# Performance work log

Hardware: AMD Instinct MI355X
Metric: run time of the kernel (lower is better)

The kernel has to match this reference:

```python
import jax, jax.numpy as jnp
import numpy as np

N_NODES = 100000


def _hetero_block(x, ei_t, ei_i, Wt, bt, Wi, bi, Wr, br):
    """ResidualGeneralHeteroConvBlock: per-edge-type linear message passing,
    'add' aggregation for temp_previous, 'mean' for intersects, summed across
    edge types, plus linear residual, ReLU."""
    n = x.shape[0]
    # transform-then-gather (cheaper than per-edge transform)
    ht = x @ Wt + bt                                   # [N, C]
    hi = x @ Wi + bi                                   # [N, C]
    # temp_previous: sum aggregation over incoming edges
    agg_t = jax.ops.segment_sum(ht[ei_t[0]], ei_t[1], num_segments=n)
    # intersects: mean aggregation
    sum_i = jax.ops.segment_sum(hi[ei_i[0]], ei_i[1], num_segments=n)
    cnt = jax.ops.segment_sum(jnp.ones((ei_i.shape[1],), x.dtype), ei_i[1],
                              num_segments=n)
    agg_i = sum_i / jnp.maximum(cnt, 1.0)[:, None]
    return jax.nn.relu(agg_t + agg_i + (x @ Wr + br))


def setup_inputs() -> dict:
    key = jax.random.key(0)
    ks = jax.random.split(key, 12)
    E = 2000000
    d = {
        "x": jax.random.normal(ks[0], (N_NODES, 6), jnp.float32),
        "edge_index_temp": jax.random.randint(ks[1], (2, E), 0, N_NODES),
        "edge_index_inter": jax.random.randint(ks[2], (2, E), 0, N_NODES),
        "W1t": jax.random.normal(ks[3], (6, 32), jnp.float32) * 0.3,
        "b1t": jnp.zeros((32,), jnp.float32),
        "W1i": jax.random.normal(ks[4], (6, 32), jnp.float32) * 0.3,
        "b1i": jnp.zeros((32,), jnp.float32),
        "W1r": jax.random.normal(ks[5], (6, 32), jnp.float32) * 0.3,
        "b1r": jnp.zeros((32,), jnp.float32),
        "W2t": jax.random.normal(ks[6], (32, 32), jnp.float32) * 0.15,
        "b2t": jnp.zeros((32,), jnp.float32),
        "W2i": jax.random.normal(ks[7], (32, 32), jnp.float32) * 0.15,
        "b2i": jnp.zeros((32,), jnp.float32),
        "W2r": jax.random.normal(ks[8], (32, 32), jnp.float32) * 0.15,
        "b2r": jnp.zeros((32,), jnp.float32),
        "Wc": jax.random.normal(ks[9], (32, 7), jnp.float32) * 0.15,
        "bc": jnp.zeros((7,), jnp.float32),
    }
    return d


def reference(x, edge_index_temp, edge_index_inter,
              W1t, b1t, W1i, b1i, W1r, b1r,
              W2t, b2t, W2i, b2i, W2r, b2r, Wc, bc):
    h = _hetero_block(x, edge_index_temp, edge_index_inter,
                      W1t, b1t, W1i, b1i, W1r, b1r)
    h = _hetero_block(h, edge_index_temp, edge_index_inter,
                      W2t, b2t, W2i, b2i, W2r, b2r)
    return h @ Wc + bc  # [N, num_classes]
```

## Files before the change

### kernel.cpp

```cpp
#include <hip/hip_runtime.h>


#define BLK 256
#define RN 512
#define KMAX 256
#define CAP 11264
#define CHUNK 4096

typedef unsigned short us8 __attribute__((ext_vector_type(8)));

__device__ inline unsigned short f2bf(float f) {
  unsigned u = __float_as_uint(f);
  return (unsigned short)((u + 0x7FFFu + ((u >> 16) & 1u)) >> 16);
}
__device__ inline float bf2f(unsigned short h) {
  return __uint_as_float(((unsigned)h) << 16);
}

__global__ __launch_bounds__(BLK) void k_prep(const float* __restrict__ x,
                                              unsigned short* __restrict__ xp,
                                              int* __restrict__ curT,
                                              int* __restrict__ curI, int N,
                                              int K) {
  int gid = blockIdx.x * BLK + threadIdx.x;
  if (gid < K) {
    curT[gid] = gid * CAP;
    curI[gid] = gid * CAP;
  }
  if (gid >= N * 8) return;
  int n = gid >> 3, c = gid & 7;
  xp[gid] = (c < 6) ? f2bf(x[n * 6 + c]) : (unsigned short)0;
}

__global__ __launch_bounds__(BLK) void k_bin3(
    const int* __restrict__ eiT, int ET, int* __restrict__ curT,
    int* __restrict__ binT, const int* __restrict__ eiI, int EI,
    int* __restrict__ curI, int* __restrict__ binI, int K) {
  const int* ei = blockIdx.y ? eiI : eiT;
  int E = blockIdx.y ? EI : ET;
  int* gcur = blockIdx.y ? curI : curT;
  int* binned = blockIdx.y ? binI : binT;
  int cs = blockIdx.x * CHUNK;
  if (cs >= E) return;
  int ce = min(E, cs + CHUNK);
  int cnt = ce - cs;
  __shared__ int ebuf[CHUNK];
  __shared__ unsigned char bbuf[CHUNK];
  __shared__ int hist[KMAX], cur[KMAX], gdelta[KMAX], s[KMAX];
  int t = threadIdx.x;
  hist[t] = 0;
  __syncthreads();
  for (int e = cs + t; e < ce; e += BLK) atomicAdd(&hist[ei[E + e] >> 9], 1);
  __syncthreads();
  int v = hist[t];
  s[t] = v;
  __syncthreads();
  for (int off = 1; off < KMAX; off <<= 1) {
    int x = (t >= off) ? s[t - off] : 0;
    __syncthreads();
    s[t] += x;
    __syncthreads();
  }
  int excl = s[t] - v;
  cur[t] = excl;
  if (t < K) gdelta[t] = atomicAdd(&gcur[t], v) - excl;
  __syncthreads();
  for (int e = cs + t; e < ce; e += BLK) {
    int src = ei[e];
    int d = ei[E + e];
    int b = d >> 9;
    int slot = atomicAdd(&cur[b], 1);
    ebuf[slot] = (src << 9) | (d & 511);
    bbuf[slot] = (unsigned char)b;
  }
  __syncthreads();
  for (int i = t; i < cnt; i += BLK) {
    int b = bbuf[i];
    __builtin_nontemporal_store(ebuf[i], &binned[i + gdelta[b]]);
  }
}

__global__ __launch_bounds__(512) void k_sortcsr2m(
    const int* __restrict__ binT, const int* __restrict__ curT,
    unsigned short* __restrict__ csrT, int* __restrict__ startT,
    int* __restrict__ degT, int* __restrict__ midT,
    const int* __restrict__ binI, const int* __restrict__ curI,
    unsigned short* __restrict__ csrI, int* __restrict__ startI,
    int* __restrict__ degI, int* __restrict__ midI, int N, int halfN) {
  const int* bin = blockIdx.y ? binI : binT;
  const int* cur = blockIdx.y ? curI : curT;
  unsigned short* csr = blockIdx.y ? csrI : csrT;
  int* start = blockIdx.y ? startI : startT;
  int* deg = blockIdx.y ? degI : degT;
  int* mid = blockIdx.y ? midI : midT;
  __shared__ int h[2 * RN], s[RN], c2[2 * RN];
  int t = threadIdx.x, b = blockIdx.x;
  int e0 = b * CAP;
  int cnt = min(cur[b] - e0, CAP);
  h[t] = 0;
  h[t + RN] = 0;
  __syncthreads();
  for (int i = t; i < cnt; i += 512) {
    int p = bin[e0 + i];
    int key = ((p & 511) << 1) | ((p >> 9) >= halfN ? 1 : 0);
    atomicAdd(&h[key], 1);
  }
  __syncthreads();
  int lo = h[2 * t], hi = h[2 * t + 1];
  int pair = lo + hi;
  s[t] = pair;
  __syncthreads();
  for (int off = 1; off < 512; off <<= 1) {
    int v = (t >= off) ? s[t - off] : 0;
    __syncthreads();
    s[t] += v;
    __syncthreads();
  }
  int excl = s[t] - pair;
  c2[2 * t] = excl;
  c2[2 * t + 1] = excl + lo;
  int n = b * RN + t;
  if (n < N) {
    start[n] = e0 + excl;
    deg[n] = pair;
    mid[n] = e0 + excl + lo;
  }
  __syncthreads();
  for (int i = t; i < cnt; i += 512) {
    int p = bin[e0 + i];
    int src = p >> 9;
    int hiFlag = (src >= halfN) ? 1 : 0;
    int key = ((p & 511) << 1) | hiFlag;
    int pos = atomicAdd(&c2[key], 1);
    csr[e0 + pos] = (unsigned short)(src - hiFlag * halfN);
  }
}

#define GN1 32
__global__ __launch_bounds__(BLK) void k_g1c1(
    const unsigned short* __restrict__ xp, const float* __restrict__ x,
    const int* __restrict__ startT, const int* __restrict__ degT,
    const int* __restrict__ midT, const unsigned short* __restrict__ csrT,
    const int* __restrict__ startI, const int* __restrict__ degI,
    const int* __restrict__ midI, const unsigned short* __restrict__ csrI,
    const float* __restrict__ Wt, const float* __restrict__ bt,
    const float* __restrict__ Wi, const float* __restrict__ bi,
    const float* __restrict__ Wr, const float* __restrict__ br,
    unsigned short* __restrict__ h1b, int N, int halfN) {
  __shared__ float sGT[GN1 * 16], sGI[GN1 * 16], sx[GN1 * 6];
  __shared__ float sWt[192], sWi[192], sWr[192], sb[96];
  __shared__ float sdT[GN1], sdI[GN1];
  int t = threadIdx.x, b = blockIdx.x;
  if (t < 192) { sWt[t] = Wt[t]; sWi[t] = Wi[t]; sWr[t] = Wr[t]; }
  if (t < 32) { sb[t] = bt[t]; sb[32 + t] = bi[t]; sb[64 + t] = br[t]; }
  if (t < GN1 * 6) {
    int g = b * GN1 * 6 + t;
    sx[t] = (g < N * 6) ? x[g] : 0.0f;
  }
  int nl = t >> 3, et = (t >> 2) & 1, half = (t >> 1) & 1, sub = t & 1;
  int n = b * GN1 + nl;
  float a0 = 0.f, a1 = 0.f, a2 = 0.f, a3 = 0.f;
  int d = 0;
  if (n < N) {
    const int* startA = et ? startI : startT;
    const int* degA = et ? degI : degT;
    const int* midA = et ? midI : midT;
    const unsigned short* csrA = et ? csrI : csrT;
    int s0 = startA[n];
    d = degA[n];
    int m = midA[n];
    int i0 = half ? m : s0;
    int i1 = half ? (s0 + d) : m;
    const unsigned short* tab = xp + (half ? (size_t)halfN * 8 : 0) + sub * 4;
    int i = i0;
    for (; i + 4 <= i1; i += 4) {
      int r0 = csrA[i], r1 = csrA[i + 1], r2 = csrA[i + 2], r3 = csrA[i + 3];
      ushort4 v0 = *(const ushort4*)(tab + (size_t)r0 * 8);
      ushort4 v1 = *(const ushort4*)(tab + (size_t)r1 * 8);
      ushort4 v2 = *(const ushort4*)(tab + (size_t)r2 * 8);
      ushort4 v3 = *(const ushort4*)(tab + (size_t)r3 * 8);
      a0 += (bf2f(v0.x) + bf2f(v1.x)) + (bf2f(v2.x) + bf2f(v3.x));
      a1 += (bf2f(v0.y) + bf2f(v1.y)) + (bf2f(v2.y) + bf2f(v3.y));
      a2 += (bf2f(v0.z) + bf2f(v1.z)) + (bf2f(v2.z) + bf2f(v3.z));
      a3 += (bf2f(v0.w) + bf2f(v1.w)) + (bf2f(v2.w) + bf2f(v3.w));
    }
    for (; i < i1; ++i) {
      int r0 = csrA[i];
      ushort4 v0 = *(const ushort4*)(tab + (size_t)r0 * 8);
      a0 += bf2f(v0.x); a1 += bf2f(v0.y); a2 += bf2f(v0.z); a3 += bf2f(v0.w);
    }
  }
  float* dst = et ? sGI : sGT;
  int base = nl * 16 + half * 8 + sub * 4;
  dst[base + 0] = a0; dst[base + 1] = a1;
  dst[base + 2] = a2; dst[base + 3] = a3;
  if (half == 0 && sub == 0) {
    if (et) sdI[nl] = (float)d;
    else    sdT[nl] = (float)d;
  }
  __syncthreads();
  for (int idx = t; idx < GN1 * 32; idx += BLK) {
    int m = idx >> 5, j = idx & 31;
    int nn = b * GN1 + m;
    if (nn >= N) break;
    float fdT = sdT[m], fdI = sdI[m];
    float invI = 1.0f / fmaxf(fdI, 1.0f);
    float gate = (fdI > 0.0f) ? 1.0f : 0.0f;
    float acc = fdT * sb[j] + gate * sb[32 + j] + sb[64 + j];
#pragma unroll
    for (int k = 0; k < 6; ++k) {
      float gT = sGT[m * 16 + k] + sGT[m * 16 + 8 + k];
      float gI = sGI[m * 16 + k] + sGI[m * 16 + 8 + k];
      acc += gT * sWt[k * 32 + j];
      acc += gI * invI * sWi[k * 32 + j];
      acc += sx[m * 6 + k] * sWr[k * 32 + j];
    }
    h1b[(size_t)nn * 32 + j] = f2bf(fmaxf(acc, 0.0f));
  }
}

__device__ inline void accum8(const unsigned short* __restrict__ tab,
                              const unsigned short* __restrict__ csr, int i0,
                              int i1, float* a) {
  int i = i0;
  for (; i + 4 <= i1; i += 4) {
    int r0 = csr[i], r1 = csr[i + 1], r2 = csr[i + 2], r3 = csr[i + 3];
    us8 v0 = *(const us8*)(tab + (size_t)r0 * 32);
    us8 v1 = *(const us8*)(tab + (size_t)r1 * 32);
    us8 v2 = *(const us8*)(tab + (size_t)r2 * 32);
    us8 v3 = *(const us8*)(tab + (size_t)r3 * 32);
#pragma unroll
    for (int k = 0; k < 8; ++k)
      a[k] += (bf2f(v0[k]) + bf2f(v1[k])) + (bf2f(v2[k]) + bf2f(v3[k]));
  }
  for (; i < i1; ++i) {
    int r0 = csr[i];
    us8 v0 = *(const us8*)(tab + (size_t)r0 * 32);
#pragma unroll
    for (int k = 0; k < 8; ++k) a[k] += bf2f(v0[k]);
  }
}

__global__ __launch_bounds__(BLK) void k_gather2(
    const unsigned short* __restrict__ h1b, const int* __restrict__ startT,
    const int* __restrict__ degT, const int* __restrict__ midT,
    const unsigned short* __restrict__ csrT, const int* __restrict__ startI,
    const int* __restrict__ degI, const int* __restrict__ midI,
    const unsigned short* __restrict__ csrI, float* __restrict__ aggT,
    float* __restrict__ aggI, int N, int halfN) {
  const int* start = blockIdx.y ? startI : startT;
  const int* deg = blockIdx.y ? degI : degT;
  const int* mid = blockIdx.y ? midI : midT;
  const unsigned short* csr = blockIdx.y ? csrI : csrT;
  float* agg = blockIdx.y ? aggI : aggT;
  int gid = blockIdx.x * BLK + threadIdx.x;
  int n = gid >> 2;
  if (n >= N) return;
  int c8 = (gid & 3) * 8;
  float a[8] = {0.f, 0.f, 0.f, 0.f, 0.f, 0.f, 0.f, 0.f};
  int s0 = start[n], d = deg[n], m = mid[n];
  accum8(h1b + c8, csr, s0, m, a);
  accum8(h1b + (size_t)halfN * 32 + c8, csr, m, s0 + d, a);
  float* p = agg + (size_t)n * 32 + c8;
#pragma unroll
  for (int k = 0; k < 8; ++k) __builtin_nontemporal_store(a[k], p + k);
}

#define CN 64
__global__ __launch_bounds__(BLK) void k_combine2cls(
    const float* __restrict__ aggT, const float* __restrict__ aggI,
    const unsigned short* __restrict__ h1b, const int* __restrict__ degT,
    const int* __restrict__ degI, const float* __restrict__ Wt,
    const float* __restrict__ bt, const float* __restrict__ Wi,
    const float* __restrict__ bi, const float* __restrict__ Wr,
    const float* __restrict__ br, const float* __restrict__ Wc,
    const float* __restrict__ bc, float* __restrict__ out, int N) {
  __shared__ float hTs[CN * 32], hIs[CN * 32], hRs[CN * 32], hs2[CN * 32];
  __shared__ float sWc[224], sbc[7], sb[96];
  __shared__ float sdT[CN], sdI[CN];
  int t = threadIdx.x;
  int j = t & 31, ln = t >> 5;
  float wt[32], wi[32], wr[32];
#pragma unroll
  for (int k = 0; k < 32; ++k) {
    wt[k] = Wt[k * 32 + j];
    wi[k] = Wi[k * 32 + j];
    wr[k] = Wr[k * 32 + j];
  }
  int node0 = blockIdx.x * CN;
  size_t gbase = (size_t)node0 * 32;
  {
    const float4* sT = (const float4*)(aggT + gbase);
    const float4* sI = (const float4*)(aggI + gbase);
    ((float4*)hTs)[t] = sT[t];
    ((float4*)hTs)[t + 256] = sT[t + 256];
    ((float4*)hIs)[t] = sI[t];
    ((float4*)hIs)[t + 256] = sI[t + 256];
    us8 v = ((const us8*)(h1b + gbase))[t];
    float4 lo = {bf2f(v[0]), bf2f(v[1]), bf2f(v[2]), bf2f(v[3])};
    float4 hi = {bf2f(v[4]), bf2f(v[5]), bf2f(v[6]), bf2f(v[7])};
    ((float4*)hRs)[2 * t] = lo;
    ((float4*)hRs)[2 * t + 1] = hi;
  }
  if (t < 224) sWc[t] = Wc[t];
  if (t < 7) sbc[t] = bc[t];
  if (t < 32) { sb[t] = bt[t]; sb[32 + t] = bi[t]; sb[64 + t] = br[t]; }
  if (t < CN) {
    int n = node0 + t;
    sdT[t] = (n < N) ? (float)degT[n] : 0.f;
    sdI[t] = (n < N) ? (float)degI[n] : 0.f;
  }
  __syncthreads();
#pragma unroll
  for (int it = 0; it < CN / 8; ++it) {
    int li = it * 8 + ln;
    float dT = sdT[li], dI = sdI[li];
    float invI = 1.0f / fmaxf(dI, 1.0f);
    float gate = (dI > 0.0f) ? 1.0f : 0.0f;
    float aT = 0.f, aI = 0.f, aR = 0.f;
    const float4* hT4 = (const float4*)(hTs + li * 32);
    const float4* hI4 = (const float4*)(hIs + li * 32);
    const float4* hR4 = (const float4*)(hRs + li * 32);
#pragma unroll
    for (int kk = 0; kk < 8; ++kk) {
      float4 a = hT4[kk], bI = hI4[kk], r = hR4[kk];
      aT += a.x * wt[kk * 4 + 0] + a.y * wt[kk * 4 + 1] +
            a.z * wt[kk * 4 + 2] + a.w * wt[kk * 4 + 3];
      aI += bI.x * wi[kk * 4 + 0] + bI.y * wi[kk * 4 + 1] +
            bI.z * wi[kk * 4 + 2] + bI.w * wi[kk * 4 + 3];
      aR += r.x * wr[kk * 4 + 0] + r.y * wr[kk * 4 + 1] +
            r.z * wr[kk * 4 + 2] + r.w * wr[kk * 4 + 3];
    }
    float acc = dT * sb[j] + gate * sb[32 + j] + sb[64 + j] + aT + invI * aI + aR;
    hs2[li * 32 + j] = fmaxf(acc, 0.0f);
  }
  __syncthreads();
  if (t < 224) {
#pragma unroll
    for (int pass = 0; pass < CN * 7 / 224; ++pass) {
      int o = pass * 224 + t;
      int m = o / 7, jc = o - m * 7;
      int n = node0 + m;
      if (n < N) {
        float a = sbc[jc];
        const float* hp = hs2 + m * 32;
#pragma unroll
        for (int k = 0; k < 32; ++k) a += hp[k] * sWc[k * 7 + jc];
        out[(size_t)n * 7 + jc] = a;
      }
    }
  }
}

extern "C" void kernel_launch(void* const* d_in, const int* in_sizes, int n_in,
                              void* d_out, int out_size, void* d_ws,
                              size_t ws_size, hipStream_t stream) {
  const float* x   = (const float*)d_in[0];
  const int* ei_t  = (const int*)d_in[1];
  const int* ei_i  = (const int*)d_in[2];
  const float* W1t = (const float*)d_in[3];
  const float* b1t = (const float*)d_in[4];
  const float* W1i = (const float*)d_in[5];
  const float* b1i = (const float*)d_in[6];
  const float* W1r = (const float*)d_in[7];
  const float* b1r = (const float*)d_in[8];
  const float* W2t = (const float*)d_in[9];
  const float* b2t = (const float*)d_in[10];
  const float* W2i = (const float*)d_in[11];
  const float* b2i = (const float*)d_in[12];
  const float* W2r = (const float*)d_in[13];
  const float* b2r = (const float*)d_in[14];
  const float* Wc  = (const float*)d_in[15];
  const float* bc  = (const float*)d_in[16];
  float* out = (float*)d_out;

  const int N  = in_sizes[0] / 6;
  const int E  = in_sizes[1] / 2;
  const int Ei = in_sizes[2] / 2;
  const int K  = (N + RN - 1) / RN;
  const int halfN = N >> 1;

  float* aggT = (float*)d_ws;
  float* aggI = aggT + (size_t)N * 32;
  unsigned short* h1b = (unsigned short*)(aggI + (size_t)N * 32);
  unsigned short* xp  = h1b + (size_t)N * 32;
  int* curT   = (int*)(xp + (size_t)N * 8);
  int* curI   = curT + KMAX;
  int* startT = curI + KMAX;
  int* degT   = startT + N;
  int* midT   = degT + N;
  int* startI = midT + N;
  int* degI   = startI + N;
  int* midI   = degI + N;
  int* binT   = midI + N;
  int* binI   = binT + (size_t)K * CAP;
  unsigned short* csrT = (unsigned short*)(binI + (size_t)K * CAP);
  unsigned short* csrI = csrT + (size_t)K * CAP;

  const int gN8  = (N * 8 + BLK - 1) / BLK;
  const int gG1  = (N + GN1 - 1) / GN1;
  const int gG2  = (N * 4 + BLK - 1) / BLK;
  const int gC2  = (N + CN - 1) / CN;
  const int Emax = (E > Ei) ? E : Ei;
  const int gBin = (Emax + CHUNK - 1) / CHUNK;

  k_prep<<<gN8, BLK, 0, stream>>>(x, xp, curT, curI, N, K);
  k_bin3<<<dim3(gBin, 2), BLK, 0, stream>>>(ei_t, E, curT, binT, ei_i, Ei,
                                            curI, binI, K);
  k_sortcsr2m<<<dim3(K, 2), 512, 0, stream>>>(binT, curT, csrT, startT, degT,
                                              midT, binI, curI, csrI, startI,
                                              degI, midI, N, halfN);

  k_g1c1<<<gG1, BLK, 0, stream>>>(xp, x, startT, degT, midT, csrT, startI,
                                  degI, midI, csrI, W1t, b1t, W1i, b1i, W1r,
                                  b1r, h1b, N, halfN);

  k_gather2<<<dim3(gG2, 2), BLK, 0, stream>>>(h1b, startT, degT, midT, csrT,
                                              startI, degI, midI, csrI, aggT,
                                              aggI, N, halfN);
  k_combine2cls<<<gC2, BLK, 0, stream>>>(aggT, aggI, h1b, degT, degI, W2t,
                                         b2t, W2i, b2i, W2r, b2r, Wc, bc, out,
                                         N);
}
```

Before: 253.7 us.

## Fuse layer-2 gather with combine and classifier into one kernel

Merges the second-layer neighbor gather and the combine+classifier kernel into a single kernel. Each block of 32 nodes gathers both edge types into shared memory, then applies the W2 transforms, ReLU and classifier there. This removes the fp32 aggT/aggI intermediates (about 25 MB written and read back) and one launch. In exchange, every block reloads the three 32x32 weight matrices into shared memory, which raises per-block setup cost and LDS use and may lower occupancy.

```diff
diff --git a/kernel.cpp b/kernel.cpp
--- a/kernel.cpp
+++ b/kernel.cpp
@@ -241,113 +241,111 @@
   }
 }
 
-__global__ __launch_bounds__(BLK) void k_gather2(
-    const unsigned short* __restrict__ h1b, const int* __restrict__ startT,
-    const int* __restrict__ degT, const int* __restrict__ midT,
-    const unsigned short* __restrict__ csrT, const int* __restrict__ startI,
-    const int* __restrict__ degI, const int* __restrict__ midI,
-    const unsigned short* __restrict__ csrI, float* __restrict__ aggT,
-    float* __restrict__ aggI, int N, int halfN) {
-  const int* start = blockIdx.y ? startI : startT;
-  const int* deg = blockIdx.y ? degI : degT;
-  const int* mid = blockIdx.y ? midI : midT;
-  const unsigned short* csr = blockIdx.y ? csrI : csrT;
-  float* agg = blockIdx.y ? aggI : aggT;
-  int gid = blockIdx.x * BLK + threadIdx.x;
-  int n = gid >> 2;
-  if (n >= N) return;
-  int c8 = (gid & 3) * 8;
-  float a[8] = {0.f, 0.f, 0.f, 0.f, 0.f, 0.f, 0.f, 0.f};
-  int s0 = start[n], d = deg[n], m = mid[n];
-  accum8(h1b + c8, csr, s0, m, a);
-  accum8(h1b + (size_t)halfN * 32 + c8, csr, m, s0 + d, a);
-  float* p = agg + (size_t)n * 32 + c8;
-#pragma unroll
-  for (int k = 0; k < 8; ++k) __builtin_nontemporal_store(a[k], p + k);
-}
-
-#define CN 64
-__global__ __launch_bounds__(BLK) void k_combine2cls(
-    const float* __restrict__ aggT, const float* __restrict__ aggI,
-    const unsigned short* __restrict__ h1b, const int* __restrict__ degT,
-    const int* __restrict__ degI, const float* __restrict__ Wt,
-    const float* __restrict__ bt, const float* __restrict__ Wi,
-    const float* __restrict__ bi, const float* __restrict__ Wr,
-    const float* __restrict__ br, const float* __restrict__ Wc,
-    const float* __restrict__ bc, float* __restrict__ out, int N) {
-  __shared__ float hTs[CN * 32], hIs[CN * 32], hRs[CN * 32], hs2[CN * 32];
+#define GN2 32
+__global__ __launch_bounds__(BLK) void k_g2c2(
+    const unsigned short* __restrict__ h1b,
+    const int* __restrict__ startT, const int* __restrict__ degT,
+    const int* __restrict__ midT, const unsigned short* __restrict__ csrT,
+    const int* __restrict__ startI, const int* __restrict__ degI,
+    const int* __restrict__ midI, const unsigned short* __restrict__ csrI,
+    const float* __restrict__ Wt, const float* __restrict__ bt,
+    const float* __restrict__ Wi, const float* __restrict__ bi,
+    const float* __restrict__ Wr, const float* __restrict__ br,
+    const float* __restrict__ Wc, const float* __restrict__ bc,
+    float* __restrict__ out, int N, int halfN) {
+  __shared__ float sGT[GN2 * 32], sGI[GN2 * 32], sR[GN2 * 32], sH2[GN2 * 32];
+  __shared__ float sW2t[1024], sW2i[1024], sW2r[1024];
   __shared__ float sWc[224], sbc[7], sb[96];
-  __shared__ float sdT[CN], sdI[CN];
-  int t = threadIdx.x;
-  int j = t & 31, ln = t >> 5;
-  float wt[32], wi[32], wr[32];
-#pragma unroll
-  for (int k = 0; k < 32; ++k) {
-    wt[k] = Wt[k * 32 + j];
-    wi[k] = Wi[k * 32 + j];
-    wr[k] = Wr[k * 32 + j];
-  }
-  int node0 = blockIdx.x * CN;
-  size_t gbase = (size_t)node0 * 32;
-  {
-    const float4* sT = (const float4*)(aggT + gbase);
-    const float4* sI = (const float4*)(aggI + gbase);
-    ((float4*)hTs)[t] = sT[t];
-    ((float4*)hTs)[t + 256] = sT[t + 256];
-    ((float4*)hIs)[t] = sI[t];
-    ((float4*)hIs)[t + 256] = sI[t + 256];
-    us8 v = ((const us8*)(h1b + gbase))[t];
-    float4 lo = {bf2f(v[0]), bf2f(v[1]), bf2f(v[2]), bf2f(v[3])};
-    float4 hi = {bf2f(v[4]), bf2f(v[5]), bf2f(v[6]), bf2f(v[7])};
-    ((float4*)hRs)[2 * t] = lo;
-    ((float4*)hRs)[2 * t + 1] = hi;
+  __shared__ float sdT[GN2], sdI[GN2];
+  int t = threadIdx.x, b = blockIdx.x;
+  int node0 = b * GN2;
+  for (int i = t; i < 1024; i += BLK) {
+    sW2t[i] = Wt[i];
+    sW2i[i] = Wi[i];
+    sW2r[i] = Wr[i];
   }
   if (t < 224) sWc[t] = Wc[t];
   if (t < 7) sbc[t] = bc[t];
   if (t < 32) { sb[t] = bt[t]; sb[32 + t] = bi[t]; sb[64 + t] = br[t]; }
-  if (t < CN) {
+  if (t < GN2) {
     int n = node0 + t;
     sdT[t] = (n < N) ? (float)degT[n] : 0.f;
     sdI[t] = (n < N) ? (float)degI[n] : 0.f;
   }
-  __syncthreads();
-#pragma unroll
-  for (int it = 0; it < CN / 8; ++it) {
-    int li = it * 8 + ln;
-    float dT = sdT[li], dI = sdI[li];
-    float invI = 1.0f / fmaxf(dI, 1.0f);
-    float gate = (dI > 0.0f) ? 1.0f : 0.0f;
-    float aT = 0.f, aI = 0.f, aR = 0.f;
-    const float4* hT4 = (const float4*)(hTs + li * 32);
-    const float4* hI4 = (const float4*)(hIs + li * 32);
-    const float4* hR4 = (const float4*)(hRs + li * 32);
-#pragma unroll
-    for (int kk = 0; kk < 8; ++kk) {
-      float4 a = hT4[kk], bI = hI4[kk], r = hR4[kk];
-      aT += a.x * wt[kk * 4 + 0] + a.y * wt[kk * 4 + 1] +
-            a.z * wt[kk * 4 + 2] + a.w * wt[kk * 4 + 3];
-      aI += bI.x * wi[kk * 4 + 0] + bI.y * wi[kk * 4 + 1] +
-            bI.z * wi[kk * 4 + 2] + bI.w * wi[kk * 4 + 3];
-      aR += r.x * wr[kk * 4 + 0] + r.y * wr[kk * 4 + 1] +
-            r.z * wr[kk * 4 + 2] + r.w * wr[kk * 4 + 3];
-    }
-    float acc = dT * sb[j] + gate * sb[32 + j] + sb[64 + j] + aT + invI * aI + aR;
-    hs2[li * 32 + j] = fmaxf(acc, 0.0f);
-  }
-  __syncthreads();
-  if (t < 224) {
-#pragma unroll
-    for (int pass = 0; pass < CN * 7 / 224; ++pass) {
-      int o = pass * 224 + t;
-      int m = o / 7, jc = o - m * 7;
-      int n = node0 + m;
-      if (n < N) {
-        float a = sbc[jc];
-        const float* hp = hs2 + m * 32;
-#pragma unroll
-        for (int k = 0; k < 32; ++k) a += hp[k] * sWc[k * 7 + jc];
-        out[(size_t)n * 7 + jc] = a;
+  if (t < 128) {
+    int nn = node0 + (t >> 2);
+    if (nn < N) {
+      us8 v = ((const us8*)(h1b + (size_t)node0 * 32))[t];
+      float4 lo = {bf2f(v[0]), bf2f(v[1]), bf2f(v[2]), bf2f(v[3])};
+      float4 hi = {bf2f(v[4]), bf2f(v[5]), bf2f(v[6]), bf2f(v[7])};
+      ((float4*)sR)[2 * t] = lo;
+      ((float4*)sR)[2 * t + 1] = hi;
+    }
+  }
+  int nl = t >> 3, et = (t >> 2) & 1, q = t & 3;
+  int n = node0 + nl;
+  float a[8] = {0.f, 0.f, 0.f, 0.f, 0.f, 0.f, 0.f, 0.f};
+  if (n < N) {
+    const int* startA = et ? startI : startT;
+    const int* degA = et ? degI : degT;
+    const int* midA = et ? midI : midT;
+    const unsigned short* csrA = et ? csrI : csrT;
+    int s0 = startA[n], d = degA[n], m = midA[n];
+    accum8(h1b + q * 8, csrA, s0, m, a);
+    accum8(h1b + (size_t)halfN * 32 + q * 8, csrA, m, s0 + d, a);
+  }
+  {
+    float* dst = (et ? sGI : sGT) + nl * 32 + q * 8;
+    float4 lo = {a[0], a[1], a[2], a[3]};
+    float4 hi = {a[4], a[5], a[6], a[7]};
+    ((float4*)dst)[0] = lo;
+    ((float4*)dst)[1] = hi;
+  }
+  __syncthreads();
+  int j = t & 31;
+#pragma unroll
+  for (int p = 0; p < GN2 * 32 / BLK; ++p) {
+    int m = p * 8 + (t >> 5);
+    int nn = node0 + m;
+    if (nn < N) {
+      float dT = sdT[m], dI = sdI[m];
+      float invI = 1.0f / fmaxf(dI, 1.0f);
+      float gate = (dI > 0.0f) ? 1.0f : 0.0f;
+      float aT = 0.f, aI = 0.f, aR = 0.f;
+      const float4* gT = (const float4*)(sGT + m * 32);
+      const float4* gI = (const float4*)(sGI + m * 32);
+      const float4* gR = (const float4*)(sR + m * 32);
+#pragma unroll
+      for (int kk = 0; kk < 8; ++kk) {
+        float4 ga = gT[kk], gb = gI[kk], gr = gR[kk];
+        aT += ga.x * sW2t[(kk * 4 + 0) * 32 + j] +
+              ga.y * sW2t[(kk * 4 + 1) * 32 + j] +
+              ga.z * sW2t[(kk * 4 + 2) * 32 + j] +
+              ga.w * sW2t[(kk * 4 + 3) * 32 + j];
+        aI += gb.x * sW2i[(kk * 4 + 0) * 32 + j] +
+              gb.y * sW2i[(kk * 4 + 1) * 32 + j] +
+              gb.z * sW2i[(kk * 4 + 2) * 32 + j] +
+              gb.w * sW2i[(kk * 4 + 3) * 32 + j];
+        aR += gr.x * sW2r[(kk * 4 + 0) * 32 + j] +
+              gr.y * sW2r[(kk * 4 + 1) * 32 + j] +
+              gr.z * sW2r[(kk * 4 + 2) * 32 + j] +
+              gr.w * sW2r[(kk * 4 + 3) * 32 + j];
       }
+      float acc =
+          dT * sb[j] + gate * sb[32 + j] + sb[64 + j] + aT + invI * aI + aR;
+      sH2[m * 32 + j] = fmaxf(acc, 0.0f);
+    }
+  }
+  __syncthreads();
+  if (t < GN2 * 7) {
+    int m = t / 7, jc = t - m * 7;
+    int nn = node0 + m;
+    if (nn < N) {
+      float acc = sbc[jc];
+      const float* hp = sH2 + m * 32;
+#pragma unroll
+      for (int k = 0; k < 32; ++k) acc += hp[k] * sWc[k * 7 + jc];
+      out[(size_t)nn * 7 + jc] = acc;
     }
   }
 }
@@ -380,9 +378,7 @@
   const int K  = (N + RN - 1) / RN;
   const int halfN = N >> 1;
 
-  float* aggT = (float*)d_ws;
-  float* aggI = aggT + (size_t)N * 32;
-  unsigned short* h1b = (unsigned short*)(aggI + (size_t)N * 32);
+  unsigned short* h1b = (unsigned short*)d_ws;
   unsigned short* xp  = h1b + (size_t)N * 32;
   int* curT   = (int*)(xp + (size_t)N * 8);
   int* curI   = curT + KMAX;
@@ -399,8 +395,7 @@
 
   const int gN8  = (N * 8 + BLK - 1) / BLK;
   const int gG1  = (N + GN1 - 1) / GN1;
-  const int gG2  = (N * 4 + BLK - 1) / BLK;
-  const int gC2  = (N + CN - 1) / CN;
+  const int gG2  = (N + GN2 - 1) / GN2;
   const int Emax = (E > Ei) ? E : Ei;
   const int gBin = (Emax + CHUNK - 1) / CHUNK;
 
@@ -415,10 +410,7 @@
                                   degI, midI, csrI, W1t, b1t, W1i, b1i, W1r,
                                   b1r, h1b, N, halfN);
 
-  k_gather2<<<dim3(gG2, 2), BLK, 0, stream>>>(h1b, startT, degT, midT, csrT,
-                                              startI, degI, midI, csrI, aggT,
-                                              aggI, N, halfN);
-  k_combine2cls<<<gC2, BLK, 0, stream>>>(aggT, aggI, h1b, degT, degI, W2t,
-                                         b2t, W2i, b2i, W2r, b2r, Wc, bc, out,
-                                         N);
-}
+  k_g2c2<<<gG2, BLK, 0, stream>>>(h1b, startT, degT, midT, csrT, startI,
+                                  degI, midI, csrI, W2t, b2t, W2i, b2i, W2r,
+                                  b2r, Wc, bc, out, N, halfN);
+}
```

After: 263.4 us. 1.04x slower.

## Split CSR neighbor lists into four source-index quarters for gather locality

Applied to the files above, without the earlier changes.

The per-destination CSR sort now partitions each neighbor list by source quarter instead of source half, storing three split offsets in an int4 per node. In layer 1 each of the four threads per node/edge-type walks one quarter and loads a full 8-element bf16 row, rather than two halves with 4-element reads. Layer 2 gathers iterate over four quarter segments. The aim is to narrow the range of source rows touched at any moment so they stay in cache, at the cost of more shared-memory histogram bins and extra offset loads per node.

```diff
diff --git a/kernel.cpp b/kernel.cpp
--- a/kernel.cpp
+++ b/kernel.cpp
@@ -80,35 +80,39 @@
   }
 }
 
-__global__ __launch_bounds__(512) void k_sortcsr2m(
+__global__ __launch_bounds__(512) void k_sortcsr4(
     const int* __restrict__ binT, const int* __restrict__ curT,
     unsigned short* __restrict__ csrT, int* __restrict__ startT,
-    int* __restrict__ degT, int* __restrict__ midT,
+    int* __restrict__ degT, int4* __restrict__ mqT,
     const int* __restrict__ binI, const int* __restrict__ curI,
     unsigned short* __restrict__ csrI, int* __restrict__ startI,
-    int* __restrict__ degI, int* __restrict__ midI, int N, int halfN) {
+    int* __restrict__ degI, int4* __restrict__ mqI, int N, int qN) {
   const int* bin = blockIdx.y ? binI : binT;
   const int* cur = blockIdx.y ? curI : curT;
   unsigned short* csr = blockIdx.y ? csrI : csrT;
   int* start = blockIdx.y ? startI : startT;
   int* deg = blockIdx.y ? degI : degT;
-  int* mid = blockIdx.y ? midI : midT;
-  __shared__ int h[2 * RN], s[RN], c2[2 * RN];
+  int4* mq = blockIdx.y ? mqI : mqT;
+  __shared__ int h[4 * RN], s[RN], c2[4 * RN];
   int t = threadIdx.x, b = blockIdx.x;
   int e0 = b * CAP;
   int cnt = min(cur[b] - e0, CAP);
   h[t] = 0;
-  h[t + RN] = 0;
+  h[t + 512] = 0;
+  h[t + 1024] = 0;
+  h[t + 1536] = 0;
   __syncthreads();
   for (int i = t; i < cnt; i += 512) {
     int p = bin[e0 + i];
-    int key = ((p & 511) << 1) | ((p >> 9) >= halfN ? 1 : 0);
-    atomicAdd(&h[key], 1);
-  }
-  __syncthreads();
-  int lo = h[2 * t], hi = h[2 * t + 1];
-  int pair = lo + hi;
-  s[t] = pair;
+    int src = p >> 9;
+    int q = (src >= 2 * qN) ? ((src >= 3 * qN) ? 3 : 2)
+                            : ((src >= qN) ? 1 : 0);
+    atomicAdd(&h[((p & 511) << 2) | q], 1);
+  }
+  __syncthreads();
+  int q0 = h[4 * t], q1 = h[4 * t + 1], q2 = h[4 * t + 2], q3 = h[4 * t + 3];
+  int tot = q0 + q1 + q2 + q3;
+  s[t] = tot;
   __syncthreads();
   for (int off = 1; off < 512; off <<= 1) {
     int v = (t >= off) ? s[t - off] : 0;
@@ -116,23 +120,27 @@
     s[t] += v;
     __syncthreads();
   }
-  int excl = s[t] - pair;
-  c2[2 * t] = excl;
-  c2[2 * t + 1] = excl + lo;
+  int excl = s[t] - tot;
+  c2[4 * t] = excl;
+  c2[4 * t + 1] = excl + q0;
+  c2[4 * t + 2] = excl + q0 + q1;
+  c2[4 * t + 3] = excl + q0 + q1 + q2;
   int n = b * RN + t;
   if (n < N) {
     start[n] = e0 + excl;
-    deg[n] = pair;
-    mid[n] = e0 + excl + lo;
+    deg[n] = tot;
+    mq[n] = make_int4(e0 + excl + q0, e0 + excl + q0 + q1,
+                      e0 + excl + q0 + q1 + q2, 0);
   }
   __syncthreads();
   for (int i = t; i < cnt; i += 512) {
     int p = bin[e0 + i];
     int src = p >> 9;
-    int hiFlag = (src >= halfN) ? 1 : 0;
-    int key = ((p & 511) << 1) | hiFlag;
+    int q = (src >= 2 * qN) ? ((src >= 3 * qN) ? 3 : 2)
+                            : ((src >= qN) ? 1 : 0);
+    int key = ((p & 511) << 2) | q;
     int pos = atomicAdd(&c2[key], 1);
-    csr[e0 + pos] = (unsigned short)(src - hiFlag * halfN);
+    csr[e0 + pos] = (unsigned short)(src - q * qN);
   }
 }
 
@@ -140,14 +148,14 @@
 __global__ __launch_bounds__(BLK) void k_g1c1(
     const unsigned short* __restrict__ xp, const float* __restrict__ x,
     const int* __restrict__ startT, const int* __restrict__ degT,
-    const int* __restrict__ midT, const unsigned short* __restrict__ csrT,
+    const int4* __restrict__ mqT, const unsigned short* __restrict__ csrT,
     const int* __restrict__ startI, const int* __restrict__ degI,
-    const int* __restrict__ midI, const unsigned short* __restrict__ csrI,
+    const int4* __restrict__ mqI, const unsigned short* __restrict__ csrI,
     const float* __restrict__ Wt, const float* __restrict__ bt,
     const float* __restrict__ Wi, const float* __restrict__ bi,
     const float* __restrict__ Wr, const float* __restrict__ br,
-    unsigned short* __restrict__ h1b, int N, int halfN) {
-  __shared__ float sGT[GN1 * 16], sGI[GN1 * 16], sx[GN1 * 6];
+    unsigned short* __restrict__ h1b, int N, int qN) {
+  __shared__ float sGT[GN1 * 32], sGI[GN1 * 32], sx[GN1 * 6];
   __shared__ float sWt[192], sWi[192], sWr[192], sb[96];
   __shared__ float sdT[GN1], sdI[GN1];
   int t = threadIdx.x, b = blockIdx.x;
@@ -157,44 +165,44 @@
     int g = b * GN1 * 6 + t;
     sx[t] = (g < N * 6) ? x[g] : 0.0f;
   }
-  int nl = t >> 3, et = (t >> 2) & 1, half = (t >> 1) & 1, sub = t & 1;
+  int nl = t >> 3, et = (t >> 2) & 1, qp = t & 3;
   int n = b * GN1 + nl;
-  float a0 = 0.f, a1 = 0.f, a2 = 0.f, a3 = 0.f;
+  float a[8] = {0.f, 0.f, 0.f, 0.f, 0.f, 0.f, 0.f, 0.f};
   int d = 0;
   if (n < N) {
     const int* startA = et ? startI : startT;
     const int* degA = et ? degI : degT;
-    const int* midA = et ? midI : midT;
+    const int4* mqA = et ? mqI : mqT;
     const unsigned short* csrA = et ? csrI : csrT;
     int s0 = startA[n];
     d = degA[n];
-    int m = midA[n];
-    int i0 = half ? m : s0;
-    int i1 = half ? (s0 + d) : m;
-    const unsigned short* tab = xp + (half ? (size_t)halfN * 8 : 0) + sub * 4;
-    int i = i0;
-    for (; i + 4 <= i1; i += 4) {
+    int4 mv = mqA[n];
+    int b0 = (qp == 0) ? s0 : ((qp == 1) ? mv.x : ((qp == 2) ? mv.y : mv.z));
+    int b1 = (qp == 3) ? (s0 + d)
+                       : ((qp == 0) ? mv.x : ((qp == 1) ? mv.y : mv.z));
+    const unsigned short* tab = xp + (size_t)qp * qN * 8;
+    int i = b0;
+    for (; i + 4 <= b1; i += 4) {
       int r0 = csrA[i], r1 = csrA[i + 1], r2 = csrA[i + 2], r3 = csrA[i + 3];
-      ushort4 v0 = *(const ushort4*)(tab + (size_t)r0 * 8);
-      ushort4 v1 = *(const ushort4*)(tab + (size_t)r1 * 8);
-      ushort4 v2 = *(const ushort4*)(tab + (size_t)r2 * 8);
-      ushort4 v3 = *(const ushort4*)(tab + (size_t)r3 * 8);
-      a0 += (bf2f(v0.x) + bf2f(v1.x)) + (bf2f(v2.x) + bf2f(v3.x));
-      a1 += (bf2f(v0.y) + bf2f(v1.y)) + (bf2f(v2.y) + bf2f(v3.y));
-      a2 += (bf2f(v0.z) + bf2f(v1.z)) + (bf2f(v2.z) + bf2f(v3.z));
-      a3 += (bf2f(v0.w) + bf2f(v1.w)) + (bf2f(v2.w) + bf2f(v3.w));
+      us8 v0 = *(const us8*)(tab + (size_t)r0 * 8);
+      us8 v1 = *(const us8*)(tab + (size_t)r1 * 8);
+      us8 v2 = *(const us8*)(tab + (size_t)r2 * 8);
+      us8 v3 = *(const us8*)(tab + (size_t)r3 * 8);
+#pragma unroll
+      for (int k = 0; k < 8; ++k)
+        a[k] += (bf2f(v0[k]) + bf2f(v1[k])) + (bf2f(v2[k]) + bf2f(v3[k]));
     }
-    for (; i < i1; ++i) {
+    for (; i < b1; ++i) {
       int r0 = csrA[i];
-      ushort4 v0 = *(const ushort4*)(tab + (size_t)r0 * 8);
-      a0 += bf2f(v0.x); a1 += bf2f(v0.y); a2 += bf2f(v0.z); a3 += bf2f(v0.w);
+      us8 v0 = *(const us8*)(tab + (size_t)r0 * 8);
+#pragma unroll
+      for (int k = 0; k < 8; ++k) a[k] += bf2f(v0[k]);
     }
   }
-  float* dst = et ? sGI : sGT;
-  int base = nl * 16 + half * 8 + sub * 4;
-  dst[base + 0] = a0; dst[base + 1] = a1;
-  dst[base + 2] = a2; dst[base + 3] = a3;
-  if (half == 0 && sub == 0) {
+  float* dst = (et ? sGI : sGT) + nl * 32 + qp * 8;
+#pragma unroll
+  for (int k = 0; k < 8; ++k) dst[k] = a[k];
+  if (qp == 0) {
     if (et) sdI[nl] = (float)d;
     else    sdT[nl] = (float)d;
   }
@@ -209,8 +217,10 @@
     float acc = fdT * sb[j] + gate * sb[32 + j] + sb[64 + j];
 #pragma unroll
     for (int k = 0; k < 6; ++k) {
-      float gT = sGT[m * 16 + k] + sGT[m * 16 + 8 + k];
-      float gI = sGI[m * 16 + k] + sGI[m * 16 + 8 + k];
+      float gT = sGT[m * 32 + k] + sGT[m * 32 + 8 + k] +
+                 sGT[m * 32 + 16 + k] + sGT[m * 32 + 24 + k];
+      float gI = sGI[m * 32 + k] + sGI[m * 32 + 8 + k] +
+                 sGI[m * 32 + 16 + k] + sGI[m * 32 + 24 + k];
       acc += gT * sWt[k * 32 + j];
       acc += gI * invI * sWi[k * 32 + j];
       acc += sx[m * 6 + k] * sWr[k * 32 + j];
@@ -243,14 +253,14 @@
 
 __global__ __launch_bounds__(BLK) void k_gather2(
     const unsigned short* __restrict__ h1b, const int* __restrict__ startT,
-    const int* __restrict__ degT, const int* __restrict__ midT,
+    const int* __restrict__ degT, const int4* __restrict__ mqT,
     const unsigned short* __restrict__ csrT, const int* __restrict__ startI,
-    const int* __restrict__ degI, const int* __restrict__ midI,
+    const int* __restrict__ degI, const int4* __restrict__ mqI,
     const unsigned short* __restrict__ csrI, float* __restrict__ aggT,
-    float* __restrict__ aggI, int N, int halfN) {
+    float* __restrict__ aggI, int N, int qN) {
   const int* start = blockIdx.y ? startI : startT;
   const int* deg = blockIdx.y ? degI : degT;
-  const int* mid = blockIdx.y ? midI : midT;
+  const int4* mq = blockIdx.y ? mqI : mqT;
   const unsigned short* csr = blockIdx.y ? csrI : csrT;
   float* agg = blockIdx.y ? aggI : aggT;
   int gid = blockIdx.x * BLK + threadIdx.x;
@@ -258,9 +268,12 @@
   if (n >= N) return;
   int c8 = (gid & 3) * 8;
   float a[8] = {0.f, 0.f, 0.f, 0.f, 0.f, 0.f, 0.f, 0.f};
-  int s0 = start[n], d = deg[n], m = mid[n];
-  accum8(h1b + c8, csr, s0, m, a);
-  accum8(h1b + (size_t)halfN * 32 + c8, csr, m, s0 + d, a);
+  int s0 = start[n], d = deg[n];
+  int4 mv = mq[n];
+  accum8(h1b + c8, csr, s0, mv.x, a);
+  accum8(h1b + (size_t)qN * 32 + c8, csr, mv.x, mv.y, a);
+  accum8(h1b + (size_t)2 * qN * 32 + c8, csr, mv.y, mv.z, a);
+  accum8(h1b + (size_t)3 * qN * 32 + c8, csr, mv.z, s0 + d, a);
   float* p = agg + (size_t)n * 32 + c8;
 #pragma unroll
   for (int k = 0; k < 8; ++k) __builtin_nontemporal_store(a[k], p + k);
@@ -378,21 +391,21 @@
   const int E  = in_sizes[1] / 2;
   const int Ei = in_sizes[2] / 2;
   const int K  = (N + RN - 1) / RN;
-  const int halfN = N >> 1;
+  const int qN = (N + 3) >> 2;
 
   float* aggT = (float*)d_ws;
   float* aggI = aggT + (size_t)N * 32;
-  unsigned short* h1b = (unsigned short*)(aggI + (size_t)N * 32);
+  int4* mqT   = (int4*)(aggI + (size_t)N * 32);
+  int4* mqI   = mqT + N;
+  unsigned short* h1b = (unsigned short*)(mqI + N);
   unsigned short* xp  = h1b + (size_t)N * 32;
   int* curT   = (int*)(xp + (size_t)N * 8);
   int* curI   = curT + KMAX;
   int* startT = curI + KMAX;
   int* degT   = startT + N;
-  int* midT   = degT + N;
-  int* startI = midT + N;
+  int* startI = degT + N;
   int* degI   = startI + N;
-  int* midI   = degI + N;
-  int* binT   = midI + N;
+  int* binT   = degI + N;
   int* binI   = binT + (size_t)K * CAP;
   unsigned short* csrT = (unsigned short*)(binI + (size_t)K * CAP);
   unsigned short* csrI = csrT + (size_t)K * CAP;
@@ -407,17 +420,17 @@
   k_prep<<<gN8, BLK, 0, stream>>>(x, xp, curT, curI, N, K);
   k_bin3<<<dim3(gBin, 2), BLK, 0, stream>>>(ei_t, E, curT, binT, ei_i, Ei,
                                             curI, binI, K);
-  k_sortcsr2m<<<dim3(K, 2), 512, 0, stream>>>(binT, curT, csrT, startT, degT,
-                                              midT, binI, curI, csrI, startI,
-                                              degI, midI, N, halfN);
-
-  k_g1c1<<<gG1, BLK, 0, stream>>>(xp, x, startT, degT, midT, csrT, startI,
-                                  degI, midI, csrI, W1t, b1t, W1i, b1i, W1r,
-                                  b1r, h1b, N, halfN);
-
-  k_gather2<<<dim3(gG2, 2), BLK, 0, stream>>>(h1b, startT, degT, midT, csrT,
-                                              startI, degI, midI, csrI, aggT,
-                                              aggI, N, halfN);
+  k_sortcsr4<<<dim3(K, 2), 512, 0, stream>>>(binT, curT, csrT, startT, degT,
+                                             mqT, binI, curI, csrI, startI,
+                                             degI, mqI, N, qN);
+
+  k_g1c1<<<gG1, BLK, 0, stream>>>(xp, x, startT, degT, mqT, csrT, startI,
+                                  degI, mqI, csrI, W1t, b1t, W1i, b1i, W1r,
+                                  b1r, h1b, N, qN);
+
+  k_gather2<<<dim3(gG2, 2), BLK, 0, stream>>>(h1b, startT, degT, mqT, csrT,
+                                              startI, degI, mqI, csrI, aggT,
+                                              aggI, N, qN);
   k_combine2cls<<<gC2, BLK, 0, stream>>>(aggT, aggI, h1b, degT, degI, W2t,
                                          b2t, W2i, b2i, W2r, b2r, Wc, bc, out,
                                          N);
```

New measurement: 257.1 us. About the same (+1.3%).
